# Kernel tuning notes

Measured on AMD Instinct MI355X. Metric: run time of the kernel, lower is better.

Reference implementation:

```python
import jax, jax.numpy as jnp
import numpy as np

NEG_SLOPE = 0.2  # PyG GATConv default leaky_relu slope


def _add_self_loops(edge_index, num_nodes):
    loop = jnp.arange(num_nodes, dtype=edge_index.dtype)
    return jnp.concatenate([edge_index, jnp.stack([loop, loop])], axis=1)


def _gat_conv(x, edge_index, W, a_src, a_dst, b, heads, out_c):
    # x: [N, Fin]; W: [Fin, heads*out_c]; a_src/a_dst: [heads, out_c]; b: [heads*out_c]
    N = x.shape[0]
    h = (x @ W).reshape(N, heads, out_c)                       # [N,H,C]
    src, dst = edge_index[0], edge_index[1]
    alpha_src = jnp.einsum('nhc,hc->nh', h, a_src)             # [N,H]
    alpha_dst = jnp.einsum('nhc,hc->nh', h, a_dst)             # [N,H]
    e = jax.nn.leaky_relu(alpha_src[src] + alpha_dst[dst], NEG_SLOPE)  # [E,H]
    # segment softmax over edges grouped by destination node
    m = jax.ops.segment_max(e, dst, num_segments=N)
    m = jnp.where(jnp.isfinite(m), m, jnp.zeros_like(m))
    ex = jnp.exp(e - m[dst])
    denom = jax.ops.segment_sum(ex, dst, num_segments=N)
    alpha = ex / (denom[dst] + 1e-16)                          # [E,H]
    out = jax.ops.segment_sum(h[src] * alpha[:, :, None], dst, num_segments=N)
    return out.reshape(N, heads * out_c) + b


def setup_inputs() -> dict:
    key = jax.random.key(0)
    ks = jax.random.split(key, 16)
    N, E, FIN, HID, HEADS, OUT = 50000, 800000, 128, 32, 4, 64
    x = jax.random.normal(ks[0], (N, FIN), dtype=jnp.float32)
    edge_index = jax.random.randint(ks[1], (2, E), 0, N, dtype=jnp.int64)
    s = 0.1
    inp = {
        'x': x, 'edge_index': edge_index,
        'W0': jax.random.normal(ks[2], (FIN, HEADS * HID), jnp.float32) * s,
        'asrc0': jax.random.normal(ks[3], (HEADS, HID), jnp.float32) * s,
        'adst0': jax.random.normal(ks[4], (HEADS, HID), jnp.float32) * s,
        'b0': jnp.zeros((HEADS * HID,), jnp.float32),
        'W1': jax.random.normal(ks[5], (HEADS * HID, HEADS * HID), jnp.float32) * s,
        'asrc1': jax.random.normal(ks[6], (HEADS, HID), jnp.float32) * s,
        'adst1': jax.random.normal(ks[7], (HEADS, HID), jnp.float32) * s,
        'b1': jnp.zeros((HEADS * HID,), jnp.float32),
        'W2': jax.random.normal(ks[8], (HEADS * HID, OUT), jnp.float32) * s,
        'asrc2': jax.random.normal(ks[9], (1, OUT), jnp.float32) * s,
        'adst2': jax.random.normal(ks[10], (1, OUT), jnp.float32) * s,
        'b2': jnp.zeros((OUT,), jnp.float32),
    }
    return inp


def reference(x, edge_index, W0, asrc0, adst0, b0, W1, asrc1, adst1, b1, W2, asrc2, adst2, b2):
    # Dropout is identity in eval mode.
    N = x.shape[0]
    ei = _add_self_loops(edge_index, N)
    h = _gat_conv(x, ei, W0, asrc0, adst0, b0, heads=4, out_c=32)
    h = jax.nn.relu(h)
    h = _gat_conv(h, ei, W1, asrc1, adst1, b1, heads=4, out_c=32)
    h = jax.nn.relu(h)
    out = _gat_conv(h, ei, W2, asrc2, adst2, b2, heads=1, out_c=64)
    return out
```

## Files before the change

kernel.cpp:

```cpp
#include <hip/hip_runtime.h>


#define NEG_SLOPE 0.2f

typedef _Float16 f16;
typedef f16 f16x8 __attribute__((ext_vector_type(8)));
typedef f16 f16x4 __attribute__((ext_vector_type(4)));
typedef f16 f16x2 __attribute__((ext_vector_type(2)));
typedef float f32x4 __attribute__((ext_vector_type(4)));

__device__ __forceinline__ float lrelu(float v) { return v > 0.f ? v : NEG_SLOPE * v; }


__global__ void fill_zero_kernel(int* __restrict__ p, int n) {
    int i = blockIdx.x * blockDim.x + threadIdx.x;
    if (i < n) p[i] = 0;
}

__global__ __launch_bounds__(256) void bucket_count_kernel(const int* __restrict__ dst, int E,
                                                           int* __restrict__ bcount) {
    __shared__ int lh[256];
    lh[threadIdx.x] = 0;
    __syncthreads();
    int stride = gridDim.x * 256 * 4;
    for (int i = (blockIdx.x * 256 + threadIdx.x) * 4; i < E; i += stride) {
        int4 d = *(const int4*)&dst[i];
        atomicAdd(&lh[d.x >> 8], 1);
        atomicAdd(&lh[d.y >> 8], 1);
        atomicAdd(&lh[d.z >> 8], 1);
        atomicAdd(&lh[d.w >> 8], 1);
    }
    __syncthreads();
    int v = lh[threadIdx.x];
    if (v > 0) atomicAdd(&bcount[threadIdx.x], v);
}

__global__ __launch_bounds__(256) void bucket_scan_kernel(const int* __restrict__ bcount, int NBK,
                                                          int* __restrict__ bbase,
                                                          int* __restrict__ bcursor,
                                                          int* __restrict__ offsets, int N) {
    int t = threadIdx.x;
    int own = (t < NBK) ? bcount[t] : 0;
    int v = own;
    int lane = t & 63, wid = t >> 6;
#pragma unroll
    for (int off = 1; off < 64; off <<= 1) {
        int u = __shfl_up(v, off);
        if (lane >= off) v += u;
    }
    __shared__ int ws[4];
    if (lane == 63) ws[wid] = v;
    __syncthreads();
    int add = 0;
    for (int w = 0; w < wid; ++w) add += ws[w];
    v += add;
    int exc = v - own;
    if (t < NBK) {
        bbase[t] = exc;
        bcursor[t] = exc;
    }
    if (t == 255) {
        bbase[NBK] = v;
        offsets[N] = v;
    }
}

#define SC_TILE 4096
__global__ __launch_bounds__(256) void bucket_scatter_kernel(const int* __restrict__ src,
                                                             const int* __restrict__ dst, int E,
                                                             int* __restrict__ bcursor,
                                                             unsigned int* __restrict__ staging) {
    __shared__ int lh[256];
    __shared__ int lcur[256];
    int tid = threadIdx.x;
    lh[tid] = 0;
    __syncthreads();
    int base = blockIdx.x * SC_TILE + tid * 16;
    int sv[16], dv[16];
    bool act = base < E;
    if (act) {
#pragma unroll
        for (int q = 0; q < 4; ++q) {
            *(int4*)&sv[q * 4] = *(const int4*)&src[base + q * 4];
            *(int4*)&dv[q * 4] = *(const int4*)&dst[base + q * 4];
        }
#pragma unroll
        for (int j = 0; j < 16; ++j) atomicAdd(&lh[dv[j] >> 8], 1);
    }
    __syncthreads();
    int c = lh[tid];
    if (c > 0) lcur[tid] = atomicAdd(&bcursor[tid], c);
    __syncthreads();
    if (act) {
#pragma unroll
        for (int j = 0; j < 16; ++j) {
            int b = dv[j] >> 8;
            int pos = atomicAdd(&lcur[b], 1);
            staging[pos] = (unsigned int)sv[j] | ((unsigned int)(dv[j] & 255) << 16);
        }
    }
}

__global__ __launch_bounds__(256) void bucket_sort_kernel(const unsigned int* __restrict__ staging,
                                                          const int* __restrict__ bbase,
                                                          int* __restrict__ offsets,
                                                          int* __restrict__ ssrc, int N) {
    __shared__ int lh[256];
    __shared__ int ws[4];
    int b = blockIdx.x;
    int tid = threadIdx.x;
    int s = bbase[b], e = bbase[b + 1];
    int cnt = e - s;
    lh[tid] = 0;
    __syncthreads();
    for (int i = tid; i < cnt; i += 256) atomicAdd(&lh[staging[s + i] >> 16], 1);
    __syncthreads();
    int own = lh[tid];
    int v = own;
    int lane = tid & 63, wid = tid >> 6;
#pragma unroll
    for (int off = 1; off < 64; off <<= 1) {
        int u = __shfl_up(v, off);
        if (lane >= off) v += u;
    }
    if (lane == 63) ws[wid] = v;
    __syncthreads();
    int add = 0;
    for (int w = 0; w < wid; ++w) add += ws[w];
    int exc = v + add - own;
    int dstn = (b << 8) + tid;
    if (dstn < N) offsets[dstn] = s + exc;
    __syncthreads();
    lh[tid] = exc;
    __syncthreads();
    for (int i = tid; i < cnt; i += 256) {
        unsigned int rec = staging[s + i];
        int dlow = rec >> 16;
        int r = atomicAdd(&lh[dlow], 1);
        unsigned int full = (rec & 0xFFFFu) | ((unsigned int)((b << 8) | dlow) << 16);
        ssrc[s + r] = (int)full;
    }
}


__global__ void split_x_kernel(const float* __restrict__ x, f16* __restrict__ xh,
                               f16* __restrict__ xl, int total4) {
    int i = blockIdx.x * blockDim.x + threadIdx.x;
    if (i >= total4) return;
    float4 v = *(const float4*)&x[(size_t)i * 4];
    float vv[4] = {v.x, v.y, v.z, v.w};
    f16x4 h, l;
#pragma unroll
    for (int j = 0; j < 4; ++j) {
        f16 hj = (f16)vv[j];
        h[j] = hj;
        l[j] = (f16)(vv[j] - (float)hj);
    }
    *(f16x4*)&xh[(size_t)i * 4] = h;
    *(f16x4*)&xl[(size_t)i * 4] = l;
}

__global__ void split_w_kernel(const float* __restrict__ W0, const float* __restrict__ W1,
                               const float* __restrict__ W2, f16* __restrict__ w0h,
                               f16* __restrict__ w0l, f16* __restrict__ w1h,
                               f16* __restrict__ w1l, f16* __restrict__ w2h,
                               f16* __restrict__ w2l) {
    int idx = blockIdx.x * 256 + threadIdx.x;
    if (idx < 16384) {
        int k = idx >> 7, c = idx & 127;
        float v = W0[k * 128 + c];
        f16 h = (f16)v;
        w0h[c * 128 + k] = h;
        w0l[c * 128 + k] = (f16)(v - (float)h);
    } else if (idx < 32768) {
        int t = idx - 16384;
        int k = t >> 7, c = t & 127;
        float v = W1[k * 128 + c];
        f16 h = (f16)v;
        w1h[c * 128 + k] = h;
        w1l[c * 128 + k] = (f16)(v - (float)h);
    } else if (idx < 40960) {
        int t = idx - 32768;
        int k = t >> 6, c = t & 63;
        float v = W2[k * 64 + c];
        f16 h = (f16)v;
        w2h[c * 128 + k] = h;
        w2l[c * 128 + k] = (f16)(v - (float)h);
    }
}

template <int FOUT>
__global__ __launch_bounds__(256) void gemm_mfma_kernel(
    const f16* __restrict__ Ah, const f16* __restrict__ Al, const f16* __restrict__ Bh,
    const f16* __restrict__ Bl, f16* __restrict__ H16, int N) {
    constexpr int CT = FOUT / 16;
    __shared__ f16 lw[2][FOUT][72];
    int tid = threadIdx.x;
    int w = tid >> 6, lane = tid & 63;
    int quad = lane >> 4, m = lane & 15;
    int row0 = blockIdx.x * 64 + w * 16;
    int arow = row0 + m;
    if (arow >= N) arow = N - 1;
    const f16* aph = &Ah[(size_t)arow * 128 + quad * 8];
    const f16* apl = &Al[(size_t)arow * 128 + quad * 8];

    f32x4 acc[CT];
#pragma unroll
    for (int t = 0; t < CT; ++t) acc[t] = (f32x4){0.f, 0.f, 0.f, 0.f};

    for (int kh = 0; kh < 2; ++kh) {
        __syncthreads();
        for (int f = tid; f < FOUT * 8; f += 256) {
            int col = f >> 3, ch = f & 7;
            *(f16x8*)&lw[0][col][ch * 8] = *(const f16x8*)&Bh[(size_t)col * 128 + kh * 64 + ch * 8];
            *(f16x8*)&lw[1][col][ch * 8] = *(const f16x8*)&Bl[(size_t)col * 128 + kh * 64 + ch * 8];
        }
        __syncthreads();
#pragma unroll
        for (int kc = 0; kc < 2; ++kc) {
            f16x8 fah = *(const f16x8*)&aph[kh * 64 + kc * 32];
            f16x8 fal = *(const f16x8*)&apl[kh * 64 + kc * 32];
#pragma unroll
            for (int t = 0; t < CT; ++t) {
                f16x8 fbh = *(const f16x8*)&lw[0][t * 16 + m][kc * 32 + quad * 8];
                f16x8 fbl = *(const f16x8*)&lw[1][t * 16 + m][kc * 32 + quad * 8];
                acc[t] = __builtin_amdgcn_mfma_f32_16x16x32_f16(fah, fbh, acc[t], 0, 0, 0);
                acc[t] = __builtin_amdgcn_mfma_f32_16x16x32_f16(fal, fbh, acc[t], 0, 0, 0);
                acc[t] = __builtin_amdgcn_mfma_f32_16x16x32_f16(fah, fbl, acc[t], 0, 0, 0);
            }
        }
    }
#pragma unroll
    for (int r = 0; r < 4; ++r) {
        int row = row0 + quad * 4 + r;
        if (row < N) {
#pragma unroll
            for (int t = 0; t < CT; ++t)
                H16[(size_t)row * FOUT + t * 16 + m] = (f16)acc[t][r];
        }
    }
}

template <int H_, int C>
__global__ void alpha_kernel(const f16* __restrict__ h16, const float* __restrict__ a_src,
                             const float* __restrict__ a_dst, float* __restrict__ asrc,
                             float* __restrict__ adst, int N) {
    int idx = blockIdx.x * blockDim.x + threadIdx.x;
    if (idx >= N * H_) return;
    int n = idx / H_, h = idx % H_;
    const f16* hp = &h16[(size_t)n * H_ * C + h * C];
    const float* as = &a_src[h * C];
    const float* ad = &a_dst[h * C];
    float s1 = 0.f, s2 = 0.f;
#pragma unroll
    for (int c8 = 0; c8 < C / 8; ++c8) {
        f16x8 v = *(const f16x8*)&hp[c8 * 8];
#pragma unroll
        for (int j = 0; j < 8; ++j) {
            float vv = (float)v[j];
            s1 += vv * as[c8 * 8 + j];
            s2 += vv * ad[c8 * 8 + j];
        }
    }
    asrc[idx] = s1;
    adst[idx] = s2;
}

template <int H_>
__global__ void edgew_kernel(const int* __restrict__ ssrc, const float* __restrict__ asrc,
                             const float* __restrict__ adst, float* __restrict__ w, int E) {
    int k = blockIdx.x * 256 + threadIdx.x;
    if (k >= E) return;
    unsigned int rec = (unsigned int)ssrc[k];
    int s = rec & 0xFFFFu, d = rec >> 16;
    if (H_ == 4) {
        float4 a_s = *(const float4*)&asrc[s * 4];
        float4 a_dd = *(const float4*)&adst[d * 4];
        float4 a_sd = *(const float4*)&asrc[d * 4];
        float4 o;
        o.x = __expf(lrelu(a_s.x + a_dd.x) - lrelu(a_sd.x + a_dd.x));
        o.y = __expf(lrelu(a_s.y + a_dd.y) - lrelu(a_sd.y + a_dd.y));
        o.z = __expf(lrelu(a_s.z + a_dd.z) - lrelu(a_sd.z + a_dd.z));
        o.w = __expf(lrelu(a_s.w + a_dd.w) - lrelu(a_sd.w + a_dd.w));
        *(float4*)&w[(size_t)k * 4] = o;
    } else {
        w[k] = __expf(lrelu(asrc[s] + adst[d]) - lrelu(asrc[d] + adst[d]));
    }
}

template <int H_, int C, bool RELU, bool SPLIT_OUT>
__global__ __launch_bounds__(256) void aggr_kernel(
    const f16* __restrict__ h16, const float* __restrict__ wedge,
    const float* __restrict__ bias, const int* __restrict__ offsets,
    const int* __restrict__ ssrc, float* __restrict__ outf, f16* __restrict__ outh,
    f16* __restrict__ outl, int N) {
    constexpr int FOUT = H_ * C;
    constexpr int LPG = FOUT / 8;
    constexpr int GROUPS = 64 / LPG;
    constexpr int UN = (GROUPS == 4) ? 4 : 2;
    int wid = threadIdx.x >> 6;
    int lane = threadIdx.x & 63;
    int n = blockIdx.x * 4 + wid;
    if (n >= N) return;
    int g = lane / LPG;
    int t = lane % LPG;
    int c0 = t * 8;
    int head = c0 / C;

    float D = 0.f;
    float S[8];
#pragma unroll
    for (int j = 0; j < 8; ++j) S[j] = 0.f;
    if (g == 0) {
        D = 1.f;
        f16x8 hv = *(const f16x8*)&h16[n * FOUT + c0];
#pragma unroll
        for (int j = 0; j < 8; ++j) S[j] = (float)hv[j];
    }

    int e1 = offsets[n + 1];
    int k = offsets[n] + g;

    for (; k + (UN - 1) * GROUPS < e1; k += UN * GROUPS) {
        float wv[UN];
        f16x8 hvv[UN];
#pragma unroll
        for (int u = 0; u < UN; ++u) {
            int kk = k + u * GROUPS;
            int s = ssrc[kk] & 0xFFFF;
            wv[u] = (H_ == 4) ? wedge[(size_t)kk * 4 + head] : wedge[kk];
            hvv[u] = *(const f16x8*)&h16[s * FOUT + c0];
        }
#pragma unroll
        for (int u = 0; u < UN; ++u) {
            D += wv[u];
#pragma unroll
            for (int j = 0; j < 8; ++j) S[j] += wv[u] * (float)hvv[u][j];
        }
    }
    for (; k < e1; k += GROUPS) {
        int s = ssrc[k] & 0xFFFF;
        float w = (H_ == 4) ? wedge[(size_t)k * 4 + head] : wedge[k];
        f16x8 hv = *(const f16x8*)&h16[s * FOUT + c0];
        D += w;
#pragma unroll
        for (int j = 0; j < 8; ++j) S[j] += w * (float)hv[j];
    }

#pragma unroll
    for (int mask = LPG; mask < 64; mask <<= 1) {
        D += __shfl_xor(D, mask);
#pragma unroll
        for (int j = 0; j < 8; ++j) S[j] += __shfl_xor(S[j], mask);
    }

    if (g == 0) {
        float inv = 1.f / (D + 1e-16f);
        float v[8];
#pragma unroll
        for (int j = 0; j < 8; ++j) {
            v[j] = S[j] * inv + bias[c0 + j];
            if (RELU) v[j] = fmaxf(v[j], 0.f);
        }
        if (SPLIT_OUT) {
            f16x8 hh, ll;
#pragma unroll
            for (int j = 0; j < 8; ++j) {
                f16 h = (f16)v[j];
                hh[j] = h;
                ll[j] = (f16)(v[j] - (float)h);
            }
            *(f16x8*)&outh[n * FOUT + c0] = hh;
            *(f16x8*)&outl[n * FOUT + c0] = ll;
        } else {
            *(float4*)&outf[n * FOUT + c0] = make_float4(v[0], v[1], v[2], v[3]);
            *(float4*)&outf[n * FOUT + c0 + 4] = make_float4(v[4], v[5], v[6], v[7]);
        }
    }
}

extern "C" void kernel_launch(void* const* d_in, const int* in_sizes, int n_in,
                              void* d_out, int out_size, void* d_ws, size_t ws_size,
                              hipStream_t stream) {
    const float* x = (const float*)d_in[0];
    const int* ei = (const int*)d_in[1];
    const float* W0 = (const float*)d_in[2];
    const float* as0 = (const float*)d_in[3];
    const float* ad0 = (const float*)d_in[4];
    const float* b0 = (const float*)d_in[5];
    const float* W1 = (const float*)d_in[6];
    const float* as1 = (const float*)d_in[7];
    const float* ad1 = (const float*)d_in[8];
    const float* b1 = (const float*)d_in[9];
    const float* W2 = (const float*)d_in[10];
    const float* as2 = (const float*)d_in[11];
    const float* ad2 = (const float*)d_in[12];
    const float* b2 = (const float*)d_in[13];

    const int N = in_sizes[0] / 128;
    const int E = in_sizes[1] / 2;
    const int NBK = (N + 255) >> 8;

    float* aS = (float*)d_ws;
    float* aD = aS + (size_t)N * 4;
    f16* h16 = (f16*)(aD + (size_t)N * 4);
    f16* xh = h16 + (size_t)N * 128;
    f16* xl = xh + (size_t)N * 128;
    f16* w0h = xl + (size_t)N * 128;
    f16* w0l = w0h + 16384;
    f16* w1h = w0l + 16384;
    f16* w1l = w1h + 16384;
    f16* w2h = w1l + 16384;
    f16* w2l = w2h + 8192;
    int* offsets = (int*)(w2l + 8192);
    int* ssrc = offsets + N + 1;
    unsigned int* staging = (unsigned int*)(ssrc + E);
    float* wedge = (float*)(staging + E);
    int* bcount = (int*)(wedge + (size_t)E * 4);
    int* bbase = bcount + NBK;
    int* bcursor = bbase + NBK + 1;

    fill_zero_kernel<<<1, 256, 0, stream>>>(bcount, NBK);
    bucket_count_kernel<<<196, 256, 0, stream>>>(ei + E, E, bcount);
    bucket_scan_kernel<<<1, 256, 0, stream>>>(bcount, NBK, bbase, bcursor, offsets, N);
    bucket_scatter_kernel<<<(E + SC_TILE - 1) / SC_TILE, 256, 0, stream>>>(ei, ei + E, E, bcursor,
                                                                           staging);
    bucket_sort_kernel<<<NBK, 256, 0, stream>>>(staging, bbase, offsets, ssrc, N);

    split_x_kernel<<<(N * 32 + 255) / 256, 256, 0, stream>>>(x, xh, xl, N * 32);
    split_w_kernel<<<160, 256, 0, stream>>>(W0, W1, W2, w0h, w0l, w1h, w1l, w2h, w2l);

    const int gGemm = (N + 63) / 64;
    const int gAggr = (N + 3) / 4;
    const int gE = (E + 255) / 256;

    gemm_mfma_kernel<128><<<gGemm, 256, 0, stream>>>(xh, xl, w0h, w0l, h16, N);
    alpha_kernel<4, 32><<<(N * 4 + 255) / 256, 256, 0, stream>>>(h16, as0, ad0, aS, aD, N);
    edgew_kernel<4><<<gE, 256, 0, stream>>>(ssrc, aS, aD, wedge, E);
    aggr_kernel<4, 32, true, true><<<gAggr, 256, 0, stream>>>(h16, wedge, b0, offsets, ssrc,
                                                              nullptr, xh, xl, N);
    gemm_mfma_kernel<128><<<gGemm, 256, 0, stream>>>(xh, xl, w1h, w1l, h16, N);
    alpha_kernel<4, 32><<<(N * 4 + 255) / 256, 256, 0, stream>>>(h16, as1, ad1, aS, aD, N);
    edgew_kernel<4><<<gE, 256, 0, stream>>>(ssrc, aS, aD, wedge, E);
    aggr_kernel<4, 32, true, true><<<gAggr, 256, 0, stream>>>(h16, wedge, b1, offsets, ssrc,
                                                              nullptr, xh, xl, N);
    gemm_mfma_kernel<64><<<gGemm, 256, 0, stream>>>(xh, xl, w2h, w2l, h16, N);
    alpha_kernel<1, 64><<<(N + 255) / 256, 256, 0, stream>>>(h16, as2, ad2, aS, aD, N);
    edgew_kernel<1><<<gE, 256, 0, stream>>>(ssrc, aS, aD, wedge, E);
    aggr_kernel<1, 64, false, false><<<gAggr, 256, 0, stream>>>(h16, wedge, b2, offsets, ssrc,
                                                                (float*)d_out, nullptr, nullptr,
                                                                N);
}
```

Baseline: 321.0 us.

## Fuse attention logits into GEMM epilogue and edge weights into aggregation; radix-sort buckets

The per-node attention dot products now run in the MFMA GEMM epilogue using lane shuffles, which removes the separate alpha kernel. Edge weights are recomputed inside the aggregation loop from asrc/adst, which removes the edgew kernel and its E×4 float write and read. The bucket sort becomes a stable LDS radix sort over 6 passes of 4 bits, so each destination's edges come out in deterministic order. The cost is extra exp work in aggregation, extra gathers of asrc, and about 82KB of shared memory in the sort kernel, which limits how many blocks fit per CU.

```diff
diff --git a/kernel.cpp b/kernel.cpp
--- a/kernel.cpp
+++ b/kernel.cpp
@@ -101,19 +101,34 @@
     }
 }
 
+#define SORT_CAP 8192
+#define MIDX(f) ((f) + ((f) >> 4))
 __global__ __launch_bounds__(256) void bucket_sort_kernel(const unsigned int* __restrict__ staging,
                                                           const int* __restrict__ bbase,
                                                           int* __restrict__ offsets,
                                                           int* __restrict__ ssrc, int N) {
+    __shared__ unsigned int bufA[SORT_CAP];
+    __shared__ unsigned int bufB[SORT_CAP];
+    __shared__ int mat[4096 + 256];
     __shared__ int lh[256];
-    __shared__ int ws[4];
+    __shared__ int wsum[4];
     int b = blockIdx.x;
     int tid = threadIdx.x;
     int s = bbase[b], e = bbase[b + 1];
     int cnt = e - s;
+    bool fits = cnt <= SORT_CAP;
+
     lh[tid] = 0;
     __syncthreads();
-    for (int i = tid; i < cnt; i += 256) atomicAdd(&lh[staging[s + i] >> 16], 1);
+    if (fits) {
+        for (int i = tid; i < cnt; i += 256) {
+            unsigned int r = staging[s + i];
+            bufA[i] = r;
+            atomicAdd(&lh[r >> 16], 1);
+        }
+    } else {
+        for (int i = tid; i < cnt; i += 256) atomicAdd(&lh[staging[s + i] >> 16], 1);
+    }
     __syncthreads();
     int own = lh[tid];
     int v = own;
@@ -123,22 +138,81 @@
         int u = __shfl_up(v, off);
         if (lane >= off) v += u;
     }
-    if (lane == 63) ws[wid] = v;
+    if (lane == 63) wsum[wid] = v;
     __syncthreads();
     int add = 0;
-    for (int w = 0; w < wid; ++w) add += ws[w];
+    for (int w = 0; w < wid; ++w) add += wsum[w];
     int exc = v + add - own;
     int dstn = (b << 8) + tid;
     if (dstn < N) offsets[dstn] = s + exc;
     __syncthreads();
-    lh[tid] = exc;
-    __syncthreads();
-    for (int i = tid; i < cnt; i += 256) {
-        unsigned int rec = staging[s + i];
-        int dlow = rec >> 16;
-        int r = atomicAdd(&lh[dlow], 1);
-        unsigned int full = (rec & 0xFFFFu) | ((unsigned int)((b << 8) | dlow) << 16);
-        ssrc[s + r] = (int)full;
+
+    if (fits) {
+        unsigned int* in = bufA;
+        unsigned int* out = bufB;
+        int L = (cnt + 255) >> 8;
+        int i0 = tid * L;
+        int i1 = i0 + L;
+        if (i0 > cnt) i0 = cnt;
+        if (i1 > cnt) i1 = cnt;
+        for (int sh = 0; sh < 24; sh += 4) {
+            int c16[16];
+#pragma unroll
+            for (int d = 0; d < 16; ++d) c16[d] = 0;
+            for (int i = i0; i < i1; ++i) c16[(in[i] >> sh) & 15]++;
+#pragma unroll
+            for (int d = 0; d < 16; ++d) mat[MIDX(d * 256 + tid)] = c16[d];
+            __syncthreads();
+            int base = tid * 16;
+            int loc[16];
+            int ssum = 0;
+#pragma unroll
+            for (int j = 0; j < 16; ++j) {
+                loc[j] = ssum;
+                ssum += mat[MIDX(base + j)];
+            }
+            int vv = ssum;
+#pragma unroll
+            for (int off = 1; off < 64; off <<= 1) {
+                int u = __shfl_up(vv, off);
+                if (lane >= off) vv += u;
+            }
+            if (lane == 63) wsum[wid] = vv;
+            __syncthreads();
+            int add2 = 0;
+            for (int w = 0; w < wid; ++w) add2 += wsum[w];
+            int exc2 = vv + add2 - ssum;
+#pragma unroll
+            for (int j = 0; j < 16; ++j) mat[MIDX(base + j)] = exc2 + loc[j];
+            __syncthreads();
+#pragma unroll
+            for (int d = 0; d < 16; ++d) c16[d] = mat[MIDX(d * 256 + tid)];
+            for (int i = i0; i < i1; ++i) {
+                unsigned int r = in[i];
+                int d = (r >> sh) & 15;
+                out[c16[d]++] = r;
+            }
+            __syncthreads();
+            unsigned int* tmp = in;
+            in = out;
+            out = tmp;
+        }
+        for (int i = tid; i < cnt; i += 256) {
+            unsigned int r = bufA[i];
+            int dlow = (r >> 16) & 255;
+            unsigned int full = (r & 0xFFFFu) | ((unsigned int)((b << 8) | dlow) << 16);
+            ssrc[s + i] = (int)full;
+        }
+    } else {
+        lh[tid] = exc;
+        __syncthreads();
+        for (int i = tid; i < cnt; i += 256) {
+            unsigned int rec = staging[s + i];
+            int dlow = rec >> 16;
+            int r = atomicAdd(&lh[dlow], 1);
+            unsigned int full = (rec & 0xFFFFu) | ((unsigned int)((b << 8) | dlow) << 16);
+            ssrc[s + r] = (int)full;
+        }
     }
 }
 
@@ -189,11 +263,13 @@
     }
 }
 
-template <int FOUT>
+template <int FOUT, int H_>
 __global__ __launch_bounds__(256) void gemm_mfma_kernel(
     const f16* __restrict__ Ah, const f16* __restrict__ Al, const f16* __restrict__ Bh,
-    const f16* __restrict__ Bl, f16* __restrict__ H16, int N) {
+    const f16* __restrict__ Bl, const float* __restrict__ a_src, const float* __restrict__ a_dst,
+    f16* __restrict__ H16, float* __restrict__ asrc, float* __restrict__ adst, int N) {
     constexpr int CT = FOUT / 16;
+    constexpr int TPH = CT / H_;
     __shared__ f16 lw[2][FOUT][72];
     int tid = threadIdx.x;
     int w = tid >> 6, lane = tid & 63;
@@ -230,70 +306,64 @@
             }
         }
     }
+
+    float asf[CT], adf[CT];
+#pragma unroll
+    for (int t = 0; t < CT; ++t) {
+        asf[t] = a_src[t * 16 + m];
+        adf[t] = a_dst[t * 16 + m];
+    }
+
 #pragma unroll
     for (int r = 0; r < 4; ++r) {
         int row = row0 + quad * 4 + r;
+        f16 hq[CT];
+        float hr[CT];
+#pragma unroll
+        for (int t = 0; t < CT; ++t) {
+            hq[t] = (f16)acc[t][r];
+            hr[t] = (float)hq[t];
+        }
+        float pa[H_], pd[H_];
+#pragma unroll
+        for (int hh = 0; hh < H_; ++hh) {
+            pa[hh] = 0.f;
+            pd[hh] = 0.f;
+#pragma unroll
+            for (int tt = 0; tt < TPH; ++tt) {
+                int t = hh * TPH + tt;
+                pa[hh] += hr[t] * asf[t];
+                pd[hh] += hr[t] * adf[t];
+            }
+        }
+#pragma unroll
+        for (int mask = 1; mask < 16; mask <<= 1) {
+#pragma unroll
+            for (int hh = 0; hh < H_; ++hh) {
+                pa[hh] += __shfl_xor(pa[hh], mask);
+                pd[hh] += __shfl_xor(pd[hh], mask);
+            }
+        }
         if (row < N) {
 #pragma unroll
-            for (int t = 0; t < CT; ++t)
-                H16[(size_t)row * FOUT + t * 16 + m] = (f16)acc[t][r];
-        }
-    }
-}
-
-template <int H_, int C>
-__global__ void alpha_kernel(const f16* __restrict__ h16, const float* __restrict__ a_src,
-                             const float* __restrict__ a_dst, float* __restrict__ asrc,
-                             float* __restrict__ adst, int N) {
-    int idx = blockIdx.x * blockDim.x + threadIdx.x;
-    if (idx >= N * H_) return;
-    int n = idx / H_, h = idx % H_;
-    const f16* hp = &h16[(size_t)n * H_ * C + h * C];
-    const float* as = &a_src[h * C];
-    const float* ad = &a_dst[h * C];
-    float s1 = 0.f, s2 = 0.f;
-#pragma unroll
-    for (int c8 = 0; c8 < C / 8; ++c8) {
-        f16x8 v = *(const f16x8*)&hp[c8 * 8];
-#pragma unroll
-        for (int j = 0; j < 8; ++j) {
-            float vv = (float)v[j];
-            s1 += vv * as[c8 * 8 + j];
-            s2 += vv * ad[c8 * 8 + j];
-        }
-    }
-    asrc[idx] = s1;
-    adst[idx] = s2;
-}
-
-template <int H_>
-__global__ void edgew_kernel(const int* __restrict__ ssrc, const float* __restrict__ asrc,
-                             const float* __restrict__ adst, float* __restrict__ w, int E) {
-    int k = blockIdx.x * 256 + threadIdx.x;
-    if (k >= E) return;
-    unsigned int rec = (unsigned int)ssrc[k];
-    int s = rec & 0xFFFFu, d = rec >> 16;
-    if (H_ == 4) {
-        float4 a_s = *(const float4*)&asrc[s * 4];
-        float4 a_dd = *(const float4*)&adst[d * 4];
-        float4 a_sd = *(const float4*)&asrc[d * 4];
-        float4 o;
-        o.x = __expf(lrelu(a_s.x + a_dd.x) - lrelu(a_sd.x + a_dd.x));
-        o.y = __expf(lrelu(a_s.y + a_dd.y) - lrelu(a_sd.y + a_dd.y));
-        o.z = __expf(lrelu(a_s.z + a_dd.z) - lrelu(a_sd.z + a_dd.z));
-        o.w = __expf(lrelu(a_s.w + a_dd.w) - lrelu(a_sd.w + a_dd.w));
-        *(float4*)&w[(size_t)k * 4] = o;
-    } else {
-        w[k] = __expf(lrelu(asrc[s] + adst[d]) - lrelu(asrc[d] + adst[d]));
+            for (int t = 0; t < CT; ++t) H16[(size_t)row * FOUT + t * 16 + m] = hq[t];
+#pragma unroll
+            for (int hh = 0; hh < H_; ++hh) {
+                if (m == hh) {
+                    asrc[row * H_ + hh] = pa[hh];
+                    adst[row * H_ + hh] = pd[hh];
+                }
+            }
+        }
     }
 }
 
 template <int H_, int C, bool RELU, bool SPLIT_OUT>
 __global__ __launch_bounds__(256) void aggr_kernel(
-    const f16* __restrict__ h16, const float* __restrict__ wedge,
-    const float* __restrict__ bias, const int* __restrict__ offsets,
-    const int* __restrict__ ssrc, float* __restrict__ outf, f16* __restrict__ outh,
-    f16* __restrict__ outl, int N) {
+    const f16* __restrict__ h16, const float* __restrict__ asrc,
+    const float* __restrict__ adst, const float* __restrict__ bias,
+    const int* __restrict__ offsets, const int* __restrict__ ssrc, float* __restrict__ outf,
+    f16* __restrict__ outh, f16* __restrict__ outl, int N) {
     constexpr int FOUT = H_ * C;
     constexpr int LPG = FOUT / 8;
     constexpr int GROUPS = 64 / LPG;
@@ -307,6 +377,9 @@
     int c0 = t * 8;
     int head = c0 / C;
 
+    float adn = adst[n * H_ + head];
+    float esf = lrelu(asrc[n * H_ + head] + adn);
+
     float D = 0.f;
     float S[8];
 #pragma unroll
@@ -322,25 +395,27 @@
     int k = offsets[n] + g;
 
     for (; k + (UN - 1) * GROUPS < e1; k += UN * GROUPS) {
-        float wv[UN];
+        int sarr[UN];
+        float aval[UN];
         f16x8 hvv[UN];
 #pragma unroll
+        for (int u = 0; u < UN; ++u) sarr[u] = ssrc[k + u * GROUPS] & 0xFFFF;
+#pragma unroll
         for (int u = 0; u < UN; ++u) {
-            int kk = k + u * GROUPS;
-            int s = ssrc[kk] & 0xFFFF;
-            wv[u] = (H_ == 4) ? wedge[(size_t)kk * 4 + head] : wedge[kk];
-            hvv[u] = *(const f16x8*)&h16[s * FOUT + c0];
+            aval[u] = asrc[sarr[u] * H_ + head];
+            hvv[u] = *(const f16x8*)&h16[sarr[u] * FOUT + c0];
         }
 #pragma unroll
         for (int u = 0; u < UN; ++u) {
-            D += wv[u];
-#pragma unroll
-            for (int j = 0; j < 8; ++j) S[j] += wv[u] * (float)hvv[u][j];
+            float w = __expf(lrelu(aval[u] + adn) - esf);
+            D += w;
+#pragma unroll
+            for (int j = 0; j < 8; ++j) S[j] += w * (float)hvv[u][j];
         }
     }
     for (; k < e1; k += GROUPS) {
         int s = ssrc[k] & 0xFFFF;
-        float w = (H_ == 4) ? wedge[(size_t)k * 4 + head] : wedge[k];
+        float w = __expf(lrelu(asrc[s * H_ + head] + adn) - esf);
         f16x8 hv = *(const f16x8*)&h16[s * FOUT + c0];
         D += w;
 #pragma unroll
@@ -415,8 +490,7 @@
     int* offsets = (int*)(w2l + 8192);
     int* ssrc = offsets + N + 1;
     unsigned int* staging = (unsigned int*)(ssrc + E);
-    float* wedge = (float*)(staging + E);
-    int* bcount = (int*)(wedge + (size_t)E * 4);
+    int* bcount = (int*)(staging + E);
     int* bbase = bcount + NBK;
     int* bcursor = bbase + NBK + 1;
 
@@ -432,22 +506,15 @@
 
     const int gGemm = (N + 63) / 64;
     const int gAggr = (N + 3) / 4;
-    const int gE = (E + 255) / 256;
-
-    gemm_mfma_kernel<128><<<gGemm, 256, 0, stream>>>(xh, xl, w0h, w0l, h16, N);
-    alpha_kernel<4, 32><<<(N * 4 + 255) / 256, 256, 0, stream>>>(h16, as0, ad0, aS, aD, N);
-    edgew_kernel<4><<<gE, 256, 0, stream>>>(ssrc, aS, aD, wedge, E);
-    aggr_kernel<4, 32, true, true><<<gAggr, 256, 0, stream>>>(h16, wedge, b0, offsets, ssrc,
+
+    gemm_mfma_kernel<128, 4><<<gGemm, 256, 0, stream>>>(xh, xl, w0h, w0l, as0, ad0, h16, aS, aD, N);
+    aggr_kernel<4, 32, true, true><<<gAggr, 256, 0, stream>>>(h16, aS, aD, b0, offsets, ssrc,
                                                               nullptr, xh, xl, N);
-    gemm_mfma_kernel<128><<<gGemm, 256, 0, stream>>>(xh, xl, w1h, w1l, h16, N);
-    alpha_kernel<4, 32><<<(N * 4 + 255) / 256, 256, 0, stream>>>(h16, as1, ad1, aS, aD, N);
-    edgew_kernel<4><<<gE, 256, 0, stream>>>(ssrc, aS, aD, wedge, E);
-    aggr_kernel<4, 32, true, true><<<gAggr, 256, 0, stream>>>(h16, wedge, b1, offsets, ssrc,
+    gemm_mfma_kernel<128, 4><<<gGemm, 256, 0, stream>>>(xh, xl, w1h, w1l, as1, ad1, h16, aS, aD, N);
+    aggr_kernel<4, 32, true, true><<<gAggr, 256, 0, stream>>>(h16, aS, aD, b1, offsets, ssrc,
                                                               nullptr, xh, xl, N);
-    gemm_mfma_kernel<64><<<gGemm, 256, 0, stream>>>(xh, xl, w2h, w2l, h16, N);
-    alpha_kernel<1, 64><<<(N + 255) / 256, 256, 0, stream>>>(h16, as2, ad2, aS, aD, N);
-    edgew_kernel<1><<<gE, 256, 0, stream>>>(ssrc, aS, aD, wedge, E);
-    aggr_kernel<1, 64, false, false><<<gAggr, 256, 0, stream>>>(h16, wedge, b2, offsets, ssrc,
+    gemm_mfma_kernel<64, 1><<<gGemm, 256, 0, stream>>>(xh, xl, w2h, w2l, as2, ad2, h16, aS, aD, N);
+    aggr_kernel<1, 64, false, false><<<gAggr, 256, 0, stream>>>(h16, aS, aD, b2, offsets, ssrc,
                                                                 (float*)d_out, nullptr, nullptr,
                                                                 N);
 }
```

Result: no change. 318.2 us (-0.9%).
